# Optimization experiments

Hardware: AMD Instinct MI355X
Metric: run time of the kernel (lower is better)

The kernel has to match this reference:

```python
import jax, jax.numpy as jnp
import numpy as np

NUM_HEADS = 12


def setup_inputs() -> dict:
    key = jax.random.key(0)
    k1, k2, k3 = jax.random.split(key, 3)
    B, N, D = 16, 1024, 768
    x = jax.random.normal(k1, (B, N, D), dtype=jnp.float32)
    qkv_w = jax.random.normal(k2, (D, 3 * D), dtype=jnp.float32) * (1.0 / np.sqrt(D))
    proj_w = jax.random.normal(k3, (D, D), dtype=jnp.float32) * (1.0 / np.sqrt(D))
    proj_b = jnp.zeros((D,), dtype=jnp.float32)
    return {"x": x, "qkv_w": qkv_w, "proj_w": proj_w, "proj_b": proj_b}


def reference(x, qkv_w, proj_w, proj_b):
    B, N, D = x.shape
    H = NUM_HEADS
    hd = D // H
    scale = hd ** -0.5
    qkv = jnp.einsum('bnd,de->bne', x, qkv_w)
    qkv = qkv.reshape(B, N, 3, H, hd).transpose(2, 0, 3, 1, 4)
    q, k, v = qkv[0], qkv[1], qkv[2]
    # attention scores [B, H, N, N]
    attn = jnp.einsum('bhqd,bhkd->bhqk', q, k) * scale
    attn = jax.nn.softmax(attn, axis=-1)
    out = jnp.einsum('bhqk,bhkd->bhqd', attn, v)
    out = out.transpose(0, 2, 1, 3).reshape(B, N, D)
    # output projection
    return jnp.einsum('bnd,de->bne', out, proj_w) + proj_b
```

## Files before the change

### kernel.cpp

```cpp
#include <hip/hip_runtime.h>
#include <cstdint>
#include <cstddef>

typedef float f32x4 __attribute__((ext_vector_type(4)));
typedef __bf16 bf16x8 __attribute__((ext_vector_type(8)));

#define BB 16
#define SEQ 1024
#define DMODEL 768
#define NHEAD 12
#define HDIM 64
#define MTOT (BB * SEQ)
#define NQKV (3 * DMODEL)
#define NQK (2 * DMODEL)
#define QSCALE 0.18033688011112042f

static __device__ __forceinline__ unsigned short f2bf(float f) {
  unsigned int u = __builtin_bit_cast(unsigned int, f);
  u += 0x7fffu + ((u >> 16) & 1u);
  return (unsigned short)(u >> 16);
}

static __device__ __forceinline__ unsigned cvt_pk_bf16(float lo, float hi) {
  unsigned r;
  asm("v_cvt_pk_bf16_f32 %0, %1, %2" : "=v"(r) : "v"(lo), "v"(hi));
  return r;
}

static __device__ __forceinline__ void gload_lds16(const void* g, void* l) {
  __builtin_amdgcn_global_load_lds((__attribute__((address_space(1))) void*)g,
                                   (__attribute__((address_space(3))) void*)l,
                                   16, 0, 0);
}

__global__ void k_cvt_bf16(const float4* __restrict__ in, ushort4* __restrict__ out, int n4) {
  int stride = gridDim.x * blockDim.x;
  for (int i = blockIdx.x * blockDim.x + threadIdx.x; i < n4; i += stride) {
    float4 v = in[i];
    ushort4 o;
    o.x = f2bf(v.x); o.y = f2bf(v.y); o.z = f2bf(v.z); o.w = f2bf(v.w);
    out[i] = o;
  }
}

__global__ void k_transpose_bf16(const float* __restrict__ in, unsigned short* __restrict__ out,
                                 int R, int C, int scaleN) {
  __shared__ float tile[32][33];
  int tx = threadIdx.x & 31, ty = threadIdx.x >> 5;
  int c0 = blockIdx.x * 32, r0 = blockIdx.y * 32;
#pragma unroll
  for (int i = 0; i < 4; ++i)
    tile[ty + i * 8][tx] = in[(size_t)(r0 + ty + i * 8) * C + c0 + tx];
  __syncthreads();
#pragma unroll
  for (int i = 0; i < 4; ++i) {
    const int n = c0 + ty + i * 8;
    float v = tile[tx][ty + i * 8];
    if (n < scaleN) v *= QSCALE;
    out[(size_t)n * R + r0 + tx] = f2bf(v);
  }
}

template <int MODE>
__global__ __launch_bounds__(256, 2) void k_gemm_bt(
    const unsigned short* __restrict__ A, const unsigned short* __restrict__ Bt,
    int M, int N, int K,
    float* __restrict__ outF, const float* __restrict__ bias,
    unsigned short* __restrict__ QK, unsigned short* __restrict__ Vt) {
  __shared__ __align__(16) unsigned short As[128 * 64];
  __shared__ __align__(16) unsigned short Bs[256 * 64];
  const int tid = threadIdx.x;
  const int lane = tid & 63, wid = tid >> 6;
  const int ln15 = lane & 15, lh = lane >> 4;
  const int wr = wid >> 1, wc = wid & 1;
  const int m0 = blockIdx.x * 128, n0 = blockIdx.y * 256;
  f32x4 acc[4][8] = {};
  const int srow = lane >> 3;
  const int sblk = ((lane & 7) ^ srow) * 8;
  const int swz = (ln15 & 7) << 3;
  const int nk = K >> 6;

  for (int kt = 0; kt < nk; ++kt) {
    const int k0 = kt * 64;
#pragma unroll
    for (int c = 0; c < 4; ++c) {
      const int ch = wid * 4 + c;
      const int row = ch * 8 + srow;
      gload_lds16(A + (size_t)(m0 + row) * K + k0 + sblk, &As[ch * 512]);
    }
#pragma unroll
    for (int c = 0; c < 8; ++c) {
      const int ch = wid * 8 + c;
      const int row = ch * 8 + srow;
      gload_lds16(Bt + (size_t)(n0 + row) * K + k0 + sblk, &Bs[ch * 512]);
    }
    __syncthreads();
#pragma unroll
    for (int kk = 0; kk < 2; ++kk) {
      const int kc = kk * 32 + lh * 8;
      bf16x8 af[4], bfv[8];
#pragma unroll
      for (int mt = 0; mt < 4; ++mt)
        af[mt] = *reinterpret_cast<const bf16x8*>(
            &As[(wr * 64 + mt * 16 + ln15) * 64 + (kc ^ swz)]);
#pragma unroll
      for (int nn = 0; nn < 8; ++nn)
        bfv[nn] = *reinterpret_cast<const bf16x8*>(
            &Bs[(wc * 128 + nn * 16 + ln15) * 64 + (kc ^ swz)]);
#pragma unroll
      for (int mt = 0; mt < 4; ++mt)
#pragma unroll
        for (int nn = 0; nn < 8; ++nn)
          acc[mt][nn] = __builtin_amdgcn_mfma_f32_16x16x32_bf16(af[mt], bfv[nn], acc[mt][nn], 0, 0, 0);
    }
    __syncthreads();
  }

#pragma unroll
  for (int mt = 0; mt < 4; ++mt) {
#pragma unroll
    for (int nn = 0; nn < 8; ++nn) {
      const int nb = n0 + wc * 128 + nn * 16;
      const int mb = m0 + wr * 64 + mt * 16 + lh * 4;
      if (MODE == 0) {
#pragma unroll
        for (int r = 0; r < 4; ++r)
          outF[(size_t)(mb + r) * N + nb + ln15] = acc[mt][nn][r] + bias[nb + ln15];
      } else if (nb < NQK) {
#pragma unroll
        for (int r = 0; r < 4; ++r)
          QK[(size_t)(mb + r) * NQK + nb + ln15] = f2bf(acc[mt][nn][r]);
      } else {
        const int rr = nb + ln15 - NQK;
        const int h = rr >> 6, d = rr & 63;
        const int b = mb >> 10, nr0 = mb & 1023;
        ushort4 u;
        u.x = f2bf(acc[mt][nn][0]); u.y = f2bf(acc[mt][nn][1]);
        u.z = f2bf(acc[mt][nn][2]); u.w = f2bf(acc[mt][nn][3]);
        *reinterpret_cast<ushort4*>(
            &Vt[(((size_t)b * NHEAD + h) * HDIM + d) * SEQ + nr0]) = u;
      }
    }
  }
}

__global__ __launch_bounds__(512) void k_attn(
    const unsigned short* __restrict__ QKn, const unsigned short* __restrict__ Vt,
    unsigned short* __restrict__ O) {
  __shared__ __align__(16) unsigned short Ks[64 * 64];
  __shared__ __align__(16) unsigned short Vs[64 * 64];
  __shared__ __align__(16) unsigned short Ps[8][16 * 72];
  const int tid = threadIdx.x;
  const int lane = tid & 63, w = tid >> 6;
  const int ln15 = lane & 15, lh = lane >> 4;
  const int o = blockIdx.x;
  const int sid = (o & 7) * 192 + (o >> 3);
  const int qb = sid & 7;
  const int bhid = sid >> 3;
  const int h = bhid % NHEAD;
  const int b = bhid / NHEAD;
  const size_t bh = (size_t)(b * NHEAD + h);
  const unsigned short* Qbase = QKn + (size_t)(b * SEQ + qb * 128 + w * 16) * NQK + h * HDIM;
  const unsigned short* Kbase = QKn + (size_t)(b * SEQ) * NQK + DMODEL + h * HDIM;
  const unsigned short* Vbase = Vt + bh * HDIM * SEQ;

  const int srow = lane >> 3;
  const int sblk = ((lane & 7) ^ srow) * 8;
  const int swz = (ln15 & 7) << 3;

  bf16x8 aq[2];
#pragma unroll
  for (int ch = 0; ch < 2; ++ch)
    aq[ch] = *reinterpret_cast<const bf16x8*>(Qbase + (size_t)ln15 * NQK + ch * 32 + lh * 8);

  f32x4 acc[4] = {};
  float mr = -1e30f, lr = 0.f;

  for (int kb = 0; kb < SEQ / 64; ++kb) {
    {
      const int row = w * 8 + srow;
      gload_lds16(Kbase + (size_t)(kb * 64 + row) * NQK + sblk, &Ks[w * 512]);
      gload_lds16(Vbase + (size_t)row * SEQ + kb * 64 + sblk, &Vs[w * 512]);
    }
    __syncthreads();

    f32x4 s[4] = {};
    __builtin_amdgcn_s_setprio(1);
#pragma unroll
    for (int t = 0; t < 4; ++t) {
#pragma unroll
      for (int ch = 0; ch < 2; ++ch) {
        bf16x8 bk = *reinterpret_cast<const bf16x8*>(
            &Ks[(t * 16 + ln15) * 64 + ((ch * 32 + lh * 8) ^ swz)]);
        s[t] = __builtin_amdgcn_mfma_f32_16x16x32_bf16(bk, aq[ch], s[t], 0, 0, 0);
      }
    }
    __builtin_amdgcn_s_setprio(0);

    float bm;
    {
      const float a0 = fmaxf(fmaxf(s[0][0], s[0][1]), fmaxf(s[0][2], s[0][3]));
      const float a1 = fmaxf(fmaxf(s[1][0], s[1][1]), fmaxf(s[1][2], s[1][3]));
      const float a2 = fmaxf(fmaxf(s[2][0], s[2][1]), fmaxf(s[2][2], s[2][3]));
      const float a3 = fmaxf(fmaxf(s[3][0], s[3][1]), fmaxf(s[3][2], s[3][3]));
      bm = fmaxf(fmaxf(a0, a1), fmaxf(a2, a3));
    }
    bm = fmaxf(bm, __shfl_xor(bm, 16));
    bm = fmaxf(bm, __shfl_xor(bm, 32));
    const int grow = __any(bm > mr + 8.f);
    float al = 1.f;
    if (grow) {
      const float mn = fmaxf(mr, bm);
      al = __builtin_amdgcn_exp2f(mr - mn);
      mr = mn;
    }
#pragma unroll
    for (int t = 0; t < 4; ++t)
#pragma unroll
      for (int r = 0; r < 4; ++r) s[t][r] = __builtin_amdgcn_exp2f(s[t][r] - mr);
    float rs;
    {
      const float a0 = (s[0][0] + s[0][1]) + (s[0][2] + s[0][3]);
      const float a1 = (s[1][0] + s[1][1]) + (s[1][2] + s[1][3]);
      const float a2 = (s[2][0] + s[2][1]) + (s[2][2] + s[2][3]);
      const float a3 = (s[3][0] + s[3][1]) + (s[3][2] + s[3][3]);
      rs = (a0 + a1) + (a2 + a3);
    }
    rs += __shfl_xor(rs, 16);
    rs += __shfl_xor(rs, 32);
    lr = lr * al + rs;
    if (grow) {
      float alq[4];
#pragma unroll
      for (int r = 0; r < 4; ++r) alq[r] = __shfl(al, lh * 4 + r);
#pragma unroll
      for (int dt = 0; dt < 4; ++dt)
#pragma unroll
        for (int r = 0; r < 4; ++r) acc[dt][r] *= alq[r];
    }

#pragma unroll
    for (int t = 0; t < 4; ++t) {
      uint2 u;
      u.x = cvt_pk_bf16(s[t][0], s[t][1]);
      u.y = cvt_pk_bf16(s[t][2], s[t][3]);
      *reinterpret_cast<uint2*>(&Ps[w][ln15 * 72 + t * 16 + lh * 4]) = u;
    }

    bf16x8 ap[2];
#pragma unroll
    for (int ch = 0; ch < 2; ++ch)
      ap[ch] = *reinterpret_cast<const bf16x8*>(&Ps[w][ln15 * 72 + ch * 32 + lh * 8]);
    __builtin_amdgcn_s_setprio(1);
#pragma unroll
    for (int dt = 0; dt < 4; ++dt) {
#pragma unroll
      for (int ch = 0; ch < 2; ++ch) {
        bf16x8 bv = *reinterpret_cast<const bf16x8*>(
            &Vs[(dt * 16 + ln15) * 64 + ((ch * 32 + lh * 8) ^ swz)]);
        acc[dt] = __builtin_amdgcn_mfma_f32_16x16x32_bf16(ap[ch], bv, acc[dt], 0, 0, 0);
      }
    }
    __builtin_amdgcn_s_setprio(0);
    __syncthreads();
  }

  float lrq[4];
#pragma unroll
  for (int r = 0; r < 4; ++r) lrq[r] = 1.0f / __shfl(lr, lh * 4 + r);
  const int qrow = qb * 128 + w * 16 + lh * 4;
#pragma unroll
  for (int dt = 0; dt < 4; ++dt)
#pragma unroll
    for (int r = 0; r < 4; ++r)
      O[((size_t)b * SEQ + qrow + r) * DMODEL + h * 64 + dt * 16 + ln15] = f2bf(acc[dt][r] * lrq[r]);
}

extern "C" void kernel_launch(void* const* d_in, const int* in_sizes, int n_in,
                              void* d_out, int out_size, void* d_ws, size_t ws_size,
                              hipStream_t stream) {
  const float* x      = (const float*)d_in[0];
  const float* qkv_w  = (const float*)d_in[1];
  const float* proj_w = (const float*)d_in[2];
  const float* proj_b = (const float*)d_in[3];
  float* out = (float*)d_out;

  char* ws = (char*)d_ws;
  const size_t SZ_XB   = (size_t)MTOT * DMODEL * 2;
  const size_t SZ_WQT  = (size_t)NQKV * DMODEL * 2;
  const size_t SZ_WPT  = (size_t)DMODEL * DMODEL * 2;
  const size_t SZ_QK   = (size_t)MTOT * NQK * 2;
  const size_t SZ_VT   = (size_t)BB * NHEAD * HDIM * SEQ * 2;
  unsigned short* Xb   = (unsigned short*)ws;
  unsigned short* WqT  = (unsigned short*)(ws + SZ_XB);
  unsigned short* WpT  = (unsigned short*)(ws + SZ_XB + SZ_WQT);
  unsigned short* QKn  = (unsigned short*)(ws + SZ_XB + SZ_WQT + SZ_WPT);
  unsigned short* Vt   = (unsigned short*)(ws + SZ_XB + SZ_WQT + SZ_WPT + SZ_QK);
  if (ws_size < SZ_XB + SZ_WQT + SZ_WPT + SZ_QK + SZ_VT) return;

  k_cvt_bf16<<<2048, 256, 0, stream>>>((const float4*)x, (ushort4*)Xb, MTOT * DMODEL / 4);
  k_transpose_bf16<<<dim3(NQKV / 32, DMODEL / 32), 256, 0, stream>>>(qkv_w, WqT, DMODEL, NQKV, DMODEL);
  k_transpose_bf16<<<dim3(DMODEL / 32, DMODEL / 32), 256, 0, stream>>>(proj_w, WpT, DMODEL, DMODEL, 0);
  k_gemm_bt<1><<<dim3(MTOT / 128, NQKV / 256), 256, 0, stream>>>(
      Xb, WqT, MTOT, NQKV, DMODEL, nullptr, nullptr, QKn, Vt);
  k_attn<<<BB * NHEAD * 8, 512, 0, stream>>>(QKn, Vt, Xb);
  k_gemm_bt<0><<<dim3(MTOT / 128, DMODEL / 256), 256, 0, stream>>>(
      Xb, WpT, MTOT, DMODEL, DMODEL, out, proj_b, nullptr, nullptr);
}
```

Before: 202.5 us.

## Shrink GEMM tiles to 128x128 and double-buffer K/V loads in attention

The GEMM kernel moves from 128x256 to 128x128 output tiles with fewer accumulators and a higher occupancy hint, which doubles the grid and should raise per-CU occupancy. The attention kernel gains two LDS buffers for K and V, prefetching the next block while the current one is computed, and drops the trailing barrier. The smaller tiles lower arithmetic intensity and add global traffic. The prefetch overlaps load latency with compute in exchange for more shared memory per block.

```diff
diff --git a/kernel.cpp b/kernel.cpp
--- a/kernel.cpp
+++ b/kernel.cpp
@@ -62,19 +62,19 @@
 }
 
 template <int MODE>
-__global__ __launch_bounds__(256, 2) void k_gemm_bt(
+__global__ __launch_bounds__(256, 3) void k_gemm_bt(
     const unsigned short* __restrict__ A, const unsigned short* __restrict__ Bt,
     int M, int N, int K,
     float* __restrict__ outF, const float* __restrict__ bias,
     unsigned short* __restrict__ QK, unsigned short* __restrict__ Vt) {
   __shared__ __align__(16) unsigned short As[128 * 64];
-  __shared__ __align__(16) unsigned short Bs[256 * 64];
+  __shared__ __align__(16) unsigned short Bs[128 * 64];
   const int tid = threadIdx.x;
   const int lane = tid & 63, wid = tid >> 6;
   const int ln15 = lane & 15, lh = lane >> 4;
   const int wr = wid >> 1, wc = wid & 1;
-  const int m0 = blockIdx.x * 128, n0 = blockIdx.y * 256;
-  f32x4 acc[4][8] = {};
+  const int m0 = blockIdx.x * 128, n0 = blockIdx.y * 128;
+  f32x4 acc[4][4] = {};
   const int srow = lane >> 3;
   const int sblk = ((lane & 7) ^ srow) * 8;
   const int swz = (ln15 & 7) << 3;
@@ -87,30 +87,25 @@
       const int ch = wid * 4 + c;
       const int row = ch * 8 + srow;
       gload_lds16(A + (size_t)(m0 + row) * K + k0 + sblk, &As[ch * 512]);
-    }
-#pragma unroll
-    for (int c = 0; c < 8; ++c) {
-      const int ch = wid * 8 + c;
-      const int row = ch * 8 + srow;
       gload_lds16(Bt + (size_t)(n0 + row) * K + k0 + sblk, &Bs[ch * 512]);
     }
     __syncthreads();
 #pragma unroll
     for (int kk = 0; kk < 2; ++kk) {
       const int kc = kk * 32 + lh * 8;
-      bf16x8 af[4], bfv[8];
+      bf16x8 af[4], bfv[4];
 #pragma unroll
       for (int mt = 0; mt < 4; ++mt)
         af[mt] = *reinterpret_cast<const bf16x8*>(
             &As[(wr * 64 + mt * 16 + ln15) * 64 + (kc ^ swz)]);
 #pragma unroll
-      for (int nn = 0; nn < 8; ++nn)
+      for (int nn = 0; nn < 4; ++nn)
         bfv[nn] = *reinterpret_cast<const bf16x8*>(
-            &Bs[(wc * 128 + nn * 16 + ln15) * 64 + (kc ^ swz)]);
+            &Bs[(wc * 64 + nn * 16 + ln15) * 64 + (kc ^ swz)]);
 #pragma unroll
       for (int mt = 0; mt < 4; ++mt)
 #pragma unroll
-        for (int nn = 0; nn < 8; ++nn)
+        for (int nn = 0; nn < 4; ++nn)
           acc[mt][nn] = __builtin_amdgcn_mfma_f32_16x16x32_bf16(af[mt], bfv[nn], acc[mt][nn], 0, 0, 0);
     }
     __syncthreads();
@@ -119,8 +114,8 @@
 #pragma unroll
   for (int mt = 0; mt < 4; ++mt) {
 #pragma unroll
-    for (int nn = 0; nn < 8; ++nn) {
-      const int nb = n0 + wc * 128 + nn * 16;
+    for (int nn = 0; nn < 4; ++nn) {
+      const int nb = n0 + wc * 64 + nn * 16;
       const int mb = m0 + wr * 64 + mt * 16 + lh * 4;
       if (MODE == 0) {
 #pragma unroll
@@ -147,8 +142,8 @@
 __global__ __launch_bounds__(512) void k_attn(
     const unsigned short* __restrict__ QKn, const unsigned short* __restrict__ Vt,
     unsigned short* __restrict__ O) {
-  __shared__ __align__(16) unsigned short Ks[64 * 64];
-  __shared__ __align__(16) unsigned short Vs[64 * 64];
+  __shared__ __align__(16) unsigned short Ks[2][64 * 64];
+  __shared__ __align__(16) unsigned short Vs[2][64 * 64];
   __shared__ __align__(16) unsigned short Ps[8][16 * 72];
   const int tid = threadIdx.x;
   const int lane = tid & 63, w = tid >> 6;
@@ -168,6 +163,12 @@
   const int sblk = ((lane & 7) ^ srow) * 8;
   const int swz = (ln15 & 7) << 3;
 
+  auto stage = [&](int kb, int s) {
+    const int row = w * 8 + srow;
+    gload_lds16(Kbase + (size_t)(kb * 64 + row) * NQK + sblk, &Ks[s][w * 512]);
+    gload_lds16(Vbase + (size_t)row * SEQ + kb * 64 + sblk, &Vs[s][w * 512]);
+  };
+
   bf16x8 aq[2];
 #pragma unroll
   for (int ch = 0; ch < 2; ++ch)
@@ -176,33 +177,31 @@
   f32x4 acc[4] = {};
   float mr = -1e30f, lr = 0.f;
 
+  stage(0, 0);
   for (int kb = 0; kb < SEQ / 64; ++kb) {
-    {
-      const int row = w * 8 + srow;
-      gload_lds16(Kbase + (size_t)(kb * 64 + row) * NQK + sblk, &Ks[w * 512]);
-      gload_lds16(Vbase + (size_t)row * SEQ + kb * 64 + sblk, &Vs[w * 512]);
-    }
+    const int s = kb & 1;
     __syncthreads();
-
-    f32x4 s[4] = {};
+    if (kb + 1 < SEQ / 64) stage(kb + 1, s ^ 1);
+
+    f32x4 sv[4] = {};
     __builtin_amdgcn_s_setprio(1);
 #pragma unroll
     for (int t = 0; t < 4; ++t) {
 #pragma unroll
       for (int ch = 0; ch < 2; ++ch) {
         bf16x8 bk = *reinterpret_cast<const bf16x8*>(
-            &Ks[(t * 16 + ln15) * 64 + ((ch * 32 + lh * 8) ^ swz)]);
-        s[t] = __builtin_amdgcn_mfma_f32_16x16x32_bf16(bk, aq[ch], s[t], 0, 0, 0);
+            &Ks[s][(t * 16 + ln15) * 64 + ((ch * 32 + lh * 8) ^ swz)]);
+        sv[t] = __builtin_amdgcn_mfma_f32_16x16x32_bf16(bk, aq[ch], sv[t], 0, 0, 0);
       }
     }
     __builtin_amdgcn_s_setprio(0);
 
     float bm;
     {
-      const float a0 = fmaxf(fmaxf(s[0][0], s[0][1]), fmaxf(s[0][2], s[0][3]));
-      const float a1 = fmaxf(fmaxf(s[1][0], s[1][1]), fmaxf(s[1][2], s[1][3]));
-      const float a2 = fmaxf(fmaxf(s[2][0], s[2][1]), fmaxf(s[2][2], s[2][3]));
-      const float a3 = fmaxf(fmaxf(s[3][0], s[3][1]), fmaxf(s[3][2], s[3][3]));
+      const float a0 = fmaxf(fmaxf(sv[0][0], sv[0][1]), fmaxf(sv[0][2], sv[0][3]));
+      const float a1 = fmaxf(fmaxf(sv[1][0], sv[1][1]), fmaxf(sv[1][2], sv[1][3]));
+      const float a2 = fmaxf(fmaxf(sv[2][0], sv[2][1]), fmaxf(sv[2][2], sv[2][3]));
+      const float a3 = fmaxf(fmaxf(sv[3][0], sv[3][1]), fmaxf(sv[3][2], sv[3][3]));
       bm = fmaxf(fmaxf(a0, a1), fmaxf(a2, a3));
     }
     bm = fmaxf(bm, __shfl_xor(bm, 16));
@@ -217,13 +216,13 @@
 #pragma unroll
     for (int t = 0; t < 4; ++t)
 #pragma unroll
-      for (int r = 0; r < 4; ++r) s[t][r] = __builtin_amdgcn_exp2f(s[t][r] - mr);
+      for (int r = 0; r < 4; ++r) sv[t][r] = __builtin_amdgcn_exp2f(sv[t][r] - mr);
     float rs;
     {
-      const float a0 = (s[0][0] + s[0][1]) + (s[0][2] + s[0][3]);
-      const float a1 = (s[1][0] + s[1][1]) + (s[1][2] + s[1][3]);
-      const float a2 = (s[2][0] + s[2][1]) + (s[2][2] + s[2][3]);
-      const float a3 = (s[3][0] + s[3][1]) + (s[3][2] + s[3][3]);
+      const float a0 = (sv[0][0] + sv[0][1]) + (sv[0][2] + sv[0][3]);
+      const float a1 = (sv[1][0] + sv[1][1]) + (sv[1][2] + sv[1][3]);
+      const float a2 = (sv[2][0] + sv[2][1]) + (sv[2][2] + sv[2][3]);
+      const float a3 = (sv[3][0] + sv[3][1]) + (sv[3][2] + sv[3][3]);
       rs = (a0 + a1) + (a2 + a3);
     }
     rs += __shfl_xor(rs, 16);
@@ -242,8 +241,8 @@
 #pragma unroll
     for (int t = 0; t < 4; ++t) {
       uint2 u;
-      u.x = cvt_pk_bf16(s[t][0], s[t][1]);
-      u.y = cvt_pk_bf16(s[t][2], s[t][3]);
+      u.x = cvt_pk_bf16(sv[t][0], sv[t][1]);
+      u.y = cvt_pk_bf16(sv[t][2], sv[t][3]);
       *reinterpret_cast<uint2*>(&Ps[w][ln15 * 72 + t * 16 + lh * 4]) = u;
     }
 
@@ -257,12 +256,11 @@
 #pragma unroll
       for (int ch = 0; ch < 2; ++ch) {
         bf16x8 bv = *reinterpret_cast<const bf16x8*>(
-            &Vs[(dt * 16 + ln15) * 64 + ((ch * 32 + lh * 8) ^ swz)]);
+            &Vs[s][(dt * 16 + ln15) * 64 + ((ch * 32 + lh * 8) ^ swz)]);
         acc[dt] = __builtin_amdgcn_mfma_f32_16x16x32_bf16(ap[ch], bv, acc[dt], 0, 0, 0);
       }
     }
     __builtin_amdgcn_s_setprio(0);
-    __syncthreads();
   }
 
   float lrq[4];
@@ -301,9 +299,9 @@
   k_cvt_bf16<<<2048, 256, 0, stream>>>((const float4*)x, (ushort4*)Xb, MTOT * DMODEL / 4);
   k_transpose_bf16<<<dim3(NQKV / 32, DMODEL / 32), 256, 0, stream>>>(qkv_w, WqT, DMODEL, NQKV, DMODEL);
   k_transpose_bf16<<<dim3(DMODEL / 32, DMODEL / 32), 256, 0, stream>>>(proj_w, WpT, DMODEL, DMODEL, 0);
-  k_gemm_bt<1><<<dim3(MTOT / 128, NQKV / 256), 256, 0, stream>>>(
+  k_gemm_bt<1><<<dim3(MTOT / 128, NQKV / 128), 256, 0, stream>>>(
       Xb, WqT, MTOT, NQKV, DMODEL, nullptr, nullptr, QKn, Vt);
   k_attn<<<BB * NHEAD * 8, 512, 0, stream>>>(QKn, Vt, Xb);
-  k_gemm_bt<0><<<dim3(MTOT / 128, DMODEL / 256), 256, 0, stream>>>(
+  k_gemm_bt<0><<<dim3(MTOT / 128, DMODEL / 128), 256, 0, stream>>>(
       Xb, WpT, MTOT, DMODEL, DMODEL, out, proj_b, nullptr, nullptr);
 }
```

After: 186.1 us. 1.09x faster.
